# Kernel tuning notes

Hardware: AMD Instinct MI355X
Metric: run time of the kernel (lower is better)

## Reference

```python
import jax, jax.numpy as jnp
import numpy as np


def setup_inputs() -> dict:
    key = jax.random.key(0)
    k1, k2 = jax.random.split(key)
    N, A, B, C = 512, 1024, 64, 16
    x = jax.random.normal(k1, (N, A), dtype=jnp.float32)
    T = jax.random.normal(k2, (A, B, C), dtype=jnp.float32)
    return {"x": x, "T": T}


def reference(x, T):
    # x: (N, A); T: (A, B, C)
    N = x.shape[0]
    A, B, C = T.shape
    # M_i = T * f(x_i)  -> (N, B, C)
    M = (x @ T.reshape(A, B * C)).reshape(N, B, C)
    # pairwise L1 distance over C: (N, N, B)
    l1 = jnp.abs(M[:, None, :, :] - M[None, :, :, :]).sum(axis=-1)
    # o(x_i)_b = sum_j exp(-||M_ib - M_jb||_1) ; subtract 1 for j == i term
    out = jnp.exp(-l1).sum(axis=1) - 1.0  # (N, B)
    return jnp.concatenate([x, out], axis=1)  # (N, A + B)
```

## Files before the change

### kernel.cpp

```cpp
#include <hip/hip_runtime.h>
#include <hip/hip_bf16.h>
#include <math.h>

#define N_   512
#define A_   1024
#define B_   64
#define C_   16
#define NBC  1024
#define OUTW 1088

#define NSCALE (-0.02254211681280365f)

typedef __attribute__((ext_vector_type(8))) short short8;
typedef __attribute__((ext_vector_type(4))) float floatx4;

__device__ __forceinline__ unsigned short f2bf_rne(float f) {
  union { float f; unsigned u; } v; v.f = f;
  unsigned r = v.u + 0x7FFFu + ((v.u >> 16) & 1u);
  return (unsigned short)(r >> 16);
}

#if __has_builtin(__builtin_amdgcn_exp2f)
__device__ __forceinline__ float exp2_hw(float x) { return __builtin_amdgcn_exp2f(x); }
#else
__device__ __forceinline__ float exp2_hw(float x) {
  float r; asm("v_exp_f32 %0, %1" : "=v"(r) : "v"(x)); return r;
}
#endif

#if __has_builtin(__builtin_amdgcn_sad_u16)
__device__ __forceinline__ unsigned sad16(unsigned a, unsigned b, unsigned c) {
  return __builtin_amdgcn_sad_u16(a, b, c);
}
#else
__device__ __forceinline__ unsigned sad16(unsigned a, unsigned b, unsigned c) {
  unsigned d; asm("v_sad_u16 %0, %1, %2, %3" : "=v"(d) : "v"(a), "v"(b), "v"(c));
  return d;
}
#endif

__global__ __launch_bounds__(256) void prep_kernel(const float* __restrict__ x,
                                                   const float* __restrict__ W,
                                                   float* __restrict__ out,
                                                   unsigned short* __restrict__ xb,
                                                   unsigned short* __restrict__ wt) {
  __shared__ float tile[64][65];
  int bid = blockIdx.x, tid = threadIdx.x;
  if (bid < 128) {
    const float4* x4 = (const float4*)x;
    float4* out4 = (float4*)out;
    int idx = bid * 256 + tid;
    #pragma unroll
    for (int rep = 0; rep < 4; ++rep, idx += 32768) {
      int row = idx >> 8, c4 = idx & 255;
      float4 f = x4[idx];
      out4[row * (OUTW / 4) + c4] = f;
      ushort4 u;
      u.x = f2bf_rne(f.x); u.y = f2bf_rne(f.y);
      u.z = f2bf_rne(f.z); u.w = f2bf_rne(f.w);
      *(ushort4*)(xb + (size_t)idx * 4) = u;
    }
  } else {
    int tb = bid - 128;
    int k0 = (tb & 15) * 64, n0 = (tb >> 4) * 64;
    int tx = tid & 63, ty = tid >> 6;
    #pragma unroll
    for (int r = ty; r < 64; r += 4)
      tile[r][tx] = W[(k0 + r) * NBC + n0 + tx];
    __syncthreads();
    #pragma unroll
    for (int r = ty; r < 64; r += 4)
      wt[(size_t)(n0 + r) * A_ + k0 + tx] = f2bf_rne(tile[tx][r]);
  }
}

__global__ __launch_bounds__(64) void gemm_kernel(const unsigned short* __restrict__ xb,
                                                  const unsigned short* __restrict__ wt,
                                                  unsigned short* __restrict__ Mq) {
  int bid  = blockIdx.x;
  int m0   = (bid & 15) * 32;
  int n0   = (bid >> 4) * 32;
  int lane = threadIdx.x;
  int lo   = lane & 15;
  int quad = lane >> 4;

  const short8* pa0 = (const short8*)(xb + (size_t)(m0 + lo) * A_ + quad * 8);
  const short8* pa1 = (const short8*)(xb + (size_t)(m0 + 16 + lo) * A_ + quad * 8);
  const short8* pb0 = (const short8*)(wt + (size_t)(n0 + lo) * A_ + quad * 8);
  const short8* pb1 = (const short8*)(wt + (size_t)(n0 + 16 + lo) * A_ + quad * 8);

  floatx4 acc00 = {0.f, 0.f, 0.f, 0.f};
  floatx4 acc01 = acc00, acc10 = acc00, acc11 = acc00;

  #pragma unroll 4
  for (int ks = 0; ks < 32; ++ks) {
    short8 a0 = pa0[ks * 4];
    short8 a1 = pa1[ks * 4];
    short8 b0 = pb0[ks * 4];
    short8 b1 = pb1[ks * 4];
    acc00 = __builtin_amdgcn_mfma_f32_16x16x32_bf16(a0, b0, acc00, 0, 0, 0);
    acc01 = __builtin_amdgcn_mfma_f32_16x16x32_bf16(a0, b1, acc01, 0, 0, 0);
    acc10 = __builtin_amdgcn_mfma_f32_16x16x32_bf16(a1, b0, acc10, 0, 0, 0);
    acc11 = __builtin_amdgcn_mfma_f32_16x16x32_bf16(a1, b1, acc11, 0, 0, 0);
  }

  int b0i = n0 >> 4;
  #pragma unroll
  for (int r = 0; r < 4; ++r) {
    int row0 = m0 + quad * 4 + r;
    int row1 = row0 + 16;
    Mq[(size_t)b0i * (N_ * C_)       + row0 * C_ + lo] = (unsigned short)(unsigned)fmaf(acc00[r], 64.f, 32768.5f);
    Mq[(size_t)(b0i + 1) * (N_ * C_) + row0 * C_ + lo] = (unsigned short)(unsigned)fmaf(acc01[r], 64.f, 32768.5f);
    Mq[(size_t)b0i * (N_ * C_)       + row1 * C_ + lo] = (unsigned short)(unsigned)fmaf(acc10[r], 64.f, 32768.5f);
    Mq[(size_t)(b0i + 1) * (N_ * C_) + row1 * C_ + lo] = (unsigned short)(unsigned)fmaf(acc11[r], 64.f, 32768.5f);
  }
}

__global__ __launch_bounds__(256) void pairwise_kernel(const unsigned short* __restrict__ Mq,
                                                       float* __restrict__ out) {
  int b   = blockIdx.x;
  int it  = blockIdx.y;
  int tid = threadIdx.x;

  __shared__ uint4 smj[1024];
  __shared__ float red[256];

  const uint4* Mb4 = (const uint4*)(Mq + (size_t)b * (N_ * C_));
  int il = tid & 31;
  int js = tid >> 5;
  int i  = it * 32 + il;

  uint4 ra = Mb4[i * 2], rb = Mb4[i * 2 + 1];

  #pragma unroll
  for (int idx = tid; idx < 1024; idx += 256)
    smj[idx] = Mb4[idx];
  __syncthreads();

  int j0 = js * 64;
  float acc = 0.f;
  #pragma unroll 2
  for (int jj = 0; jj < 64; ++jj) {
    const uint4* q4 = &smj[(j0 + jj) * 2];
    uint4 qa = q4[0], qb = q4[1];
    unsigned s0 = sad16(ra.x, qa.x, 0u);
    unsigned s1 = sad16(rb.x, qb.x, 0u);
    s0 = sad16(ra.y, qa.y, s0);
    s1 = sad16(rb.y, qb.y, s1);
    s0 = sad16(ra.z, qa.z, s0);
    s1 = sad16(rb.z, qb.z, s1);
    s0 = sad16(ra.w, qa.w, s0);
    s1 = sad16(rb.w, qb.w, s1);
    acc += exp2_hw((float)(s0 + s1) * NSCALE);
  }
  red[tid] = acc;
  __syncthreads();
  if (tid < 32) {
    float s = red[tid]       + red[tid + 32]  + red[tid + 64]  + red[tid + 96]
            + red[tid + 128] + red[tid + 160] + red[tid + 192] + red[tid + 224];
    out[(size_t)(it * 32 + tid) * OUTW + A_ + b] = s - 1.0f;
  }
}

extern "C" void kernel_launch(void* const* d_in, const int* in_sizes, int n_in,
                              void* d_out, int out_size, void* d_ws, size_t ws_size,
                              hipStream_t stream) {
  const float* x = (const float*)d_in[0];
  const float* T = (const float*)d_in[1];
  float* out = (float*)d_out;

  char* ws = (char*)d_ws;
  unsigned short* xb = (unsigned short*)(ws);
  unsigned short* wt = (unsigned short*)(ws + (1u << 20));
  unsigned short* Mq = (unsigned short*)(ws + (3u << 20));

  prep_kernel<<<dim3(384), dim3(256), 0, stream>>>(x, T, out, xb, wt);
  gemm_kernel<<<dim3(512), dim3(64), 0, stream>>>(xb, wt, Mq);
  pairwise_kernel<<<dim3(64, 16), dim3(256), 0, stream>>>(Mq, out);
}
```

Baseline: 86.46 us.

## Screen pairwise distances with 8-bit SAD before exact 16-bit evaluation

The GEMM now also writes an 8-bit coarsely quantized copy of M. The pairwise kernel uses it for a cheap SAD screen and only recomputes the exact 16-bit distance and exp for near pairs, adding them straight into the output with atomics. The prep kernel now zero-fills the output tail so these atomics can accumulate there. This skips exp work for pairs whose contribution is negligible, but it drops small terms (an approximation), excludes the self term via the s-1 test, and adds global atomics and uncoalesced re-reads for surviving pairs.

```diff
diff --git a/kernel.cpp b/kernel.cpp
--- a/kernel.cpp
+++ b/kernel.cpp
@@ -10,6 +10,8 @@
 #define OUTW 1088
 
 #define NSCALE (-0.02254211681280365f)
+#define Q8SCALE 0.6666667f
+#define SCREEN 32u
 
 typedef __attribute__((ext_vector_type(8))) short short8;
 typedef __attribute__((ext_vector_type(4))) float floatx4;
@@ -35,6 +37,17 @@
 #else
 __device__ __forceinline__ unsigned sad16(unsigned a, unsigned b, unsigned c) {
   unsigned d; asm("v_sad_u16 %0, %1, %2, %3" : "=v"(d) : "v"(a), "v"(b), "v"(c));
+  return d;
+}
+#endif
+
+#if __has_builtin(__builtin_amdgcn_sad_u8)
+__device__ __forceinline__ unsigned sad8(unsigned a, unsigned b, unsigned c) {
+  return __builtin_amdgcn_sad_u8(a, b, c);
+}
+#else
+__device__ __forceinline__ unsigned sad8(unsigned a, unsigned b, unsigned c) {
+  unsigned d; asm("v_sad_u8 %0, %1, %2, %3" : "=v"(d) : "v"(a), "v"(b), "v"(c));
   return d;
 }
 #endif
@@ -46,22 +59,27 @@
                                                    unsigned short* __restrict__ wt) {
   __shared__ float tile[64][65];
   int bid = blockIdx.x, tid = threadIdx.x;
-  if (bid < 128) {
+  if (bid < 136) {
     const float4* x4 = (const float4*)x;
     float4* out4 = (float4*)out;
-    int idx = bid * 256 + tid;
     #pragma unroll
-    for (int rep = 0; rep < 4; ++rep, idx += 32768) {
-      int row = idx >> 8, c4 = idx & 255;
-      float4 f = x4[idx];
-      out4[row * (OUTW / 4) + c4] = f;
-      ushort4 u;
-      u.x = f2bf_rne(f.x); u.y = f2bf_rne(f.y);
-      u.z = f2bf_rne(f.z); u.w = f2bf_rne(f.w);
-      *(ushort4*)(xb + (size_t)idx * 4) = u;
+    for (int rep = 0; rep < 4; ++rep) {
+      int idx = bid * 1024 + rep * 256 + tid;
+      int row = idx / (OUTW / 4);
+      int c4  = idx - row * (OUTW / 4);
+      if (c4 < (A_ / 4)) {
+        float4 f = x4[row * (A_ / 4) + c4];
+        out4[idx] = f;
+        ushort4 u;
+        u.x = f2bf_rne(f.x); u.y = f2bf_rne(f.y);
+        u.z = f2bf_rne(f.z); u.w = f2bf_rne(f.w);
+        *(ushort4*)(xb + (size_t)row * A_ + c4 * 4) = u;
+      } else {
+        out4[idx] = make_float4(0.f, 0.f, 0.f, 0.f);
+      }
     }
   } else {
-    int tb = bid - 128;
+    int tb = bid - 136;
     int k0 = (tb & 15) * 64, n0 = (tb >> 4) * 64;
     int tx = tid & 63, ty = tid >> 6;
     #pragma unroll
@@ -76,7 +94,8 @@
 
 __global__ __launch_bounds__(64) void gemm_kernel(const unsigned short* __restrict__ xb,
                                                   const unsigned short* __restrict__ wt,
-                                                  unsigned short* __restrict__ Mq) {
+                                                  unsigned short* __restrict__ Mq,
+                                                  unsigned char* __restrict__ Mq8) {
   int bid  = blockIdx.x;
   int m0   = (bid & 15) * 32;
   int n0   = (bid >> 4) * 32;
@@ -109,56 +128,56 @@
   for (int r = 0; r < 4; ++r) {
     int row0 = m0 + quad * 4 + r;
     int row1 = row0 + 16;
-    Mq[(size_t)b0i * (N_ * C_)       + row0 * C_ + lo] = (unsigned short)(unsigned)fmaf(acc00[r], 64.f, 32768.5f);
-    Mq[(size_t)(b0i + 1) * (N_ * C_) + row0 * C_ + lo] = (unsigned short)(unsigned)fmaf(acc01[r], 64.f, 32768.5f);
-    Mq[(size_t)b0i * (N_ * C_)       + row1 * C_ + lo] = (unsigned short)(unsigned)fmaf(acc10[r], 64.f, 32768.5f);
-    Mq[(size_t)(b0i + 1) * (N_ * C_) + row1 * C_ + lo] = (unsigned short)(unsigned)fmaf(acc11[r], 64.f, 32768.5f);
-  }
-}
-
-__global__ __launch_bounds__(256) void pairwise_kernel(const unsigned short* __restrict__ Mq,
+    float a00 = acc00[r], a01 = acc01[r], a10 = acc10[r], a11 = acc11[r];
+    Mq[(size_t)b0i * (N_ * C_)       + row0 * C_ + lo] = (unsigned short)(unsigned)fmaf(a00, 64.f, 32768.5f);
+    Mq[(size_t)(b0i + 1) * (N_ * C_) + row0 * C_ + lo] = (unsigned short)(unsigned)fmaf(a01, 64.f, 32768.5f);
+    Mq[(size_t)b0i * (N_ * C_)       + row1 * C_ + lo] = (unsigned short)(unsigned)fmaf(a10, 64.f, 32768.5f);
+    Mq[(size_t)(b0i + 1) * (N_ * C_) + row1 * C_ + lo] = (unsigned short)(unsigned)fmaf(a11, 64.f, 32768.5f);
+    Mq8[(size_t)b0i * (N_ * C_)       + row0 * C_ + lo] = (unsigned char)(unsigned)fminf(fmaxf(fmaf(a00, Q8SCALE, 128.5f), 0.f), 255.f);
+    Mq8[(size_t)(b0i + 1) * (N_ * C_) + row0 * C_ + lo] = (unsigned char)(unsigned)fminf(fmaxf(fmaf(a01, Q8SCALE, 128.5f), 0.f), 255.f);
+    Mq8[(size_t)b0i * (N_ * C_)       + row1 * C_ + lo] = (unsigned char)(unsigned)fminf(fmaxf(fmaf(a10, Q8SCALE, 128.5f), 0.f), 255.f);
+    Mq8[(size_t)(b0i + 1) * (N_ * C_) + row1 * C_ + lo] = (unsigned char)(unsigned)fminf(fmaxf(fmaf(a11, Q8SCALE, 128.5f), 0.f), 255.f);
+  }
+}
+
+__global__ __launch_bounds__(256) void pairwise_kernel(const unsigned char* __restrict__ Mq8,
+                                                       const unsigned short* __restrict__ Mq,
                                                        float* __restrict__ out) {
   int b   = blockIdx.x;
   int it  = blockIdx.y;
   int tid = threadIdx.x;
 
-  __shared__ uint4 smj[1024];
-  __shared__ float red[256];
-
-  const uint4* Mb4 = (const uint4*)(Mq + (size_t)b * (N_ * C_));
+  __shared__ uint4 smj[512];
+
+  const uint4* Mb8 = (const uint4*)(Mq8 + (size_t)b * (N_ * C_));
   int il = tid & 31;
   int js = tid >> 5;
   int i  = it * 32 + il;
 
-  uint4 ra = Mb4[i * 2], rb = Mb4[i * 2 + 1];
+  uint4 ra = Mb8[i];
 
   #pragma unroll
-  for (int idx = tid; idx < 1024; idx += 256)
-    smj[idx] = Mb4[idx];
+  for (int idx = tid; idx < 512; idx += 256)
+    smj[idx] = Mb8[idx];
   __syncthreads();
 
   int j0 = js * 64;
-  float acc = 0.f;
-  #pragma unroll 2
+  #pragma unroll 4
   for (int jj = 0; jj < 64; ++jj) {
-    const uint4* q4 = &smj[(j0 + jj) * 2];
-    uint4 qa = q4[0], qb = q4[1];
-    unsigned s0 = sad16(ra.x, qa.x, 0u);
-    unsigned s1 = sad16(rb.x, qb.x, 0u);
-    s0 = sad16(ra.y, qa.y, s0);
-    s1 = sad16(rb.y, qb.y, s1);
-    s0 = sad16(ra.z, qa.z, s0);
-    s1 = sad16(rb.z, qb.z, s1);
-    s0 = sad16(ra.w, qa.w, s0);
-    s1 = sad16(rb.w, qb.w, s1);
-    acc += exp2_hw((float)(s0 + s1) * NSCALE);
-  }
-  red[tid] = acc;
-  __syncthreads();
-  if (tid < 32) {
-    float s = red[tid]       + red[tid + 32]  + red[tid + 64]  + red[tid + 96]
-            + red[tid + 128] + red[tid + 160] + red[tid + 192] + red[tid + 224];
-    out[(size_t)(it * 32 + tid) * OUTW + A_ + b] = s - 1.0f;
+    uint4 q = smj[j0 + jj];
+    unsigned s = sad8(ra.x, q.x, sad8(ra.y, q.y, 0u))
+               + sad8(ra.z, q.z, sad8(ra.w, q.w, 0u));
+    if (s - 1u < SCREEN) {
+      int j = j0 + jj;
+      const uint4* pi = (const uint4*)(Mq + (size_t)b * (N_ * C_) + i * C_);
+      const uint4* pj = (const uint4*)(Mq + (size_t)b * (N_ * C_) + j * C_);
+      uint4 xa = pi[0], xb2 = pi[1], ya = pj[0], yb = pj[1];
+      unsigned t0 = sad16(xa.x, ya.x, 0u), t1 = sad16(xb2.x, yb.x, 0u);
+      t0 = sad16(xa.y, ya.y, t0);  t1 = sad16(xb2.y, yb.y, t1);
+      t0 = sad16(xa.z, ya.z, t0);  t1 = sad16(xb2.z, yb.z, t1);
+      t0 = sad16(xa.w, ya.w, t0);  t1 = sad16(xb2.w, yb.w, t1);
+      atomicAdd(&out[(size_t)i * OUTW + A_ + b], exp2_hw((float)(t0 + t1) * NSCALE));
+    }
   }
 }
 
@@ -170,11 +189,12 @@
   float* out = (float*)d_out;
 
   char* ws = (char*)d_ws;
-  unsigned short* xb = (unsigned short*)(ws);
-  unsigned short* wt = (unsigned short*)(ws + (1u << 20));
-  unsigned short* Mq = (unsigned short*)(ws + (3u << 20));
-
-  prep_kernel<<<dim3(384), dim3(256), 0, stream>>>(x, T, out, xb, wt);
-  gemm_kernel<<<dim3(512), dim3(64), 0, stream>>>(xb, wt, Mq);
-  pairwise_kernel<<<dim3(64, 16), dim3(256), 0, stream>>>(Mq, out);
-}
+  unsigned short* xb  = (unsigned short*)(ws);
+  unsigned short* wt  = (unsigned short*)(ws + (1u << 20));
+  unsigned short* Mq  = (unsigned short*)(ws + (3u << 20));
+  unsigned char*  Mq8 = (unsigned char*)(ws + (4u << 20));
+
+  prep_kernel<<<dim3(392), dim3(256), 0, stream>>>(x, T, out, xb, wt);
+  gemm_kernel<<<dim3(512), dim3(64), 0, stream>>>(xb, wt, Mq, Mq8);
+  pairwise_kernel<<<dim3(64, 16), dim3(256), 0, stream>>>(Mq8, Mq, out);
+}
```

New measurement: 80.83 us, median of 2. 1.07x faster.
